# Kernel optimization log

Measured on AMD Instinct MI355X. Metric: run time of the kernel, lower is better.

## Reference

```python
import jax, jax.numpy as jnp
import numpy as np

B, C_IN, T = 16, 1, 10240
C = 256                # conv_dim_out == config.model.conv_channels
KERNEL, STRIDE, PAD = 10, 5, 0
K_STEPS = 12           # config.model.predict_steps
NEG = 10               # config.train.neg_samples
EPS = 1e-5
L_OUT = (T + 2 * PAD - KERNEL) // STRIDE + 1   # 2047


def setup_inputs() -> dict:
    key = jax.random.key(0)
    ks = jax.random.split(key, 5)
    return {
        "x": jax.random.normal(ks[0], (B, C_IN, T), jnp.float32),
        "conv_w": jax.random.normal(ks[1], (C, C_IN, KERNEL), jnp.float32) * 0.1,
        "conv_b": jnp.zeros((C,), jnp.float32),
        "bn_gamma": jnp.ones((C,), jnp.float32),
        "bn_beta": jnp.zeros((C,), jnp.float32),
        "tr_w": jax.random.normal(ks[2], (K_STEPS, C, C), jnp.float32) / np.sqrt(C).astype(np.float32),
        "tr_b": jnp.zeros((K_STEPS, C), jnp.float32),
        "perm": jax.random.permutation(ks[3], L_OUT),  # randperm over the time axis
    }


def reference(x, conv_w, conv_b, bn_gamma, bn_beta, tr_w, tr_b, perm):
    # ---- encoder: Conv1d -> ReLU -> BatchNorm1d (training-mode batch stats) ----
    h = jax.lax.conv_general_dilated(
        x, conv_w, window_strides=(STRIDE,), padding=[(PAD, PAD)],
        dimension_numbers=("NCH", "OIH", "NCH"))
    h = jax.nn.relu(h + conv_b[None, :, None])            # (B, C, L)
    mu = h.mean(axis=(0, 2), keepdims=True)
    var = h.var(axis=(0, 2), keepdims=True)               # biased, as torch BN
    h = (h - mu) * jax.lax.rsqrt(var + EPS)
    h = h * bn_gamma[None, :, None] + bn_beta[None, :, None]
    z = h.transpose(0, 2, 1)                              # (B, L, C)

    # ---- negatives: batch-roll by 1, random permutation of the time axis; detached ----
    z_negative = jax.lax.stop_gradient(jnp.roll(z, 1, axis=0)[:, perm, :])

    L = z.shape[1]
    # z_neg_full[b, i] == roll(z_neg, i, axis=0)[b] == z_neg[(b - i) % B]
    roll_idx = (jnp.arange(B)[:, None] - jnp.arange(NEG)[None, :]) % B  # (B, NEG)

    losses = []
    for k in range(1, K_STEPS + 1):
        l_len = L - k
        z_pos = z[:, k:, :]                               # (B, l, C)
        z_neg = z_negative[:, k:, :]                      # (B, l, C)
        z_neg_full = z_neg[roll_idx]                      # (B, NEG, l, C)
        W, bb = tr_w[k - 1], tr_b[k - 1]
        est_pos = (z_pos @ W + bb)[:, None]               # (B, 1, l, C)
        est_neg = z_neg_full @ W + bb                     # (B, NEG, l, C)
        estimated = jnp.concatenate([est_pos, est_neg], axis=1)        # (B, S, l, C)
        z_full = jnp.concatenate([z_pos[:, None], z_neg_full], axis=1)  # (B, S, l, C)
        f = jnp.einsum("bslc,bslc->bsl", estimated, z_full)
        # faithful to torch: flatten (b, s, l) row-major then view as (b*l, S)
        f_k = f.reshape(B * l_len, NEG + 1)
        logp = jax.nn.log_softmax(f_k, axis=1)
        losses.append(-logp.sum() / ((l_len - k) * B))

    # torch forward returns z.permute(0, 2, 1); losses returned too for baseline use
    return z.transpose(0, 2, 1), jnp.stack(losses)
```

## Files before the change

### kernel.cpp

```cpp
#include <hip/hip_runtime.h>
#include <hip/hip_bf16.h>
#include <math.h>

constexpr int B_ = 16;
constexpr int T_ = 10240;
constexpr int C_ = 256;
constexpr int KW = 10;
constexpr int L_ = 2047;
constexpr int N_ = B_ * L_;
constexpr int KSTEPS = 12;
constexpr float EPS_ = 1e-5f;
constexpr int QSTR = 32768;

typedef short bf16x8 __attribute__((ext_vector_type(8)));
typedef float f32x4  __attribute__((ext_vector_type(4)));

__global__ __launch_bounds__(256) void stats_wt_kernel(
    const float* __restrict__ x, const float* __restrict__ cw, const float* __restrict__ cb,
    float* __restrict__ ssum, float* __restrict__ ssq,
    const float* __restrict__ tw, __hip_bfloat16* __restrict__ Wt)
{
    __shared__ float smem[64 * 65];
    const int bid = blockIdx.x;
    if (bid < 256) {
        const int b  = bid & 15;
        const int l0 = (bid >> 4) * 128;
        const int cnt = min(128, L_ - l0);
        const int c = threadIdx.x;
        float* xs = smem;
        const float* xb = x + (size_t)b * T_;
        for (int i = threadIdx.x; i < cnt * 5 + 5; i += 256) xs[i] = xb[l0 * 5 + i];
        float w[KW];
#pragma unroll
        for (int j = 0; j < KW; ++j) w[j] = cw[c * KW + j];
        const float bias = cb[c];
        __syncthreads();
        float s = 0.f, s2 = 0.f;
        for (int dl = 0; dl < cnt; ++dl) {
            float v = bias;
#pragma unroll
            for (int j = 0; j < KW; ++j) v = fmaf(xs[dl * 5 + j], w[j], v);
            v = fmaxf(v, 0.f);
            s += v;
            s2 = fmaf(v, v, s2);
        }
        atomicAdd(&ssum[c], s);
        atomicAdd(&ssq[c], s2);
    } else {
        const int idx = bid - 256;
        const int k  = idx >> 4;
        const int c0 = ((idx & 15) >> 2) * 64, j0 = (idx & 3) * 64;
        float (*tile)[65] = (float(*)[65])smem;
        for (int i = threadIdx.x; i < 64 * 64; i += 256) {
            int c = i >> 6, j = i & 63;
            tile[c][j] = tw[((size_t)k * C_ + (c0 + c)) * C_ + j0 + j];
        }
        __syncthreads();
        for (int i = threadIdx.x; i < 64 * 64; i += 256) {
            int j = i >> 6, c = i & 63;
            Wt[((size_t)k * C_ + (j0 + j)) * C_ + c0 + c] = __float2bfloat16(tile[c][j]);
        }
    }
}

__global__ void bn_finalize_kernel(const float* __restrict__ ssum, const float* __restrict__ ssq,
                                   const float* __restrict__ gamma, const float* __restrict__ beta,
                                   float* __restrict__ scale, float* __restrict__ shift)
{
    int c = threadIdx.x;
    const float inv_n = 1.0f / (float)N_;
    float mu  = ssum[c] * inv_n;
    float var = ssq[c] * inv_n - mu * mu;
    float sc  = gamma[c] * rsqrtf(var + EPS_);
    scale[c] = sc;
    shift[c] = beta[c] - mu * sc;
}

__global__ __launch_bounds__(256) void conv_norm_kernel(
    const float* __restrict__ x, const float* __restrict__ cw, const float* __restrict__ cb,
    const float* __restrict__ scale, const float* __restrict__ shift,
    __hip_bfloat16* __restrict__ Zb, float* __restrict__ out0)
{
    const int b  = blockIdx.y;
    const int l0 = blockIdx.x * 32;
    const int cnt = min(32, L_ - l0);
    const int c = threadIdx.x;
    __shared__ float xs[32 * 5 + 8];
    __shared__ float zt[32][257];
    const float* xb = x + (size_t)b * T_;
    for (int i = threadIdx.x; i < cnt * 5 + 5; i += 256) xs[i] = xb[l0 * 5 + i];
    float w[KW];
#pragma unroll
    for (int j = 0; j < KW; ++j) w[j] = cw[c * KW + j];
    const float bias = cb[c];
    const float sc = scale[c], sh = shift[c];
    __syncthreads();
    for (int dl = 0; dl < cnt; ++dl) {
        float v = bias;
#pragma unroll
        for (int j = 0; j < KW; ++j) v = fmaf(xs[dl * 5 + j], w[j], v);
        v = fmaxf(v, 0.f);
        float z = fmaf(v, sc, sh);
        Zb[((size_t)(b * L_ + l0 + dl)) * C_ + c] = __float2bfloat16(z);
        zt[dl][c] = z;
    }
    __syncthreads();
    const int lq  = threadIdx.x & 31;
    const int cr0 = threadIdx.x >> 5;
    if (lq < cnt) {
#pragma unroll
        for (int i = 0; i < 32; ++i) {
            int cr = cr0 * 32 + i;
            out0[((size_t)(b * C_ + cr)) * L_ + l0 + lq] = zt[lq][cr];
        }
    }
}

__global__ __launch_bounds__(256, 2) void qmfma_kernel(
    const __hip_bfloat16* __restrict__ Zb, const __hip_bfloat16* __restrict__ Wt,
    const float* __restrict__ tb, float* __restrict__ qt)
{
    const int k   = blockIdx.y;
    const int grp = blockIdx.x;
    const __hip_bfloat16* __restrict__ Wk = Wt + (size_t)k * C_ * C_;

    __shared__ __hip_bfloat16 zs[2][32 * 256];
    __shared__ float qacc[4][256];

    const int tid  = threadIdx.x;
    const int lane = tid & 63, wave = tid >> 6;
    const int n16  = lane & 15, quad = lane >> 4;
    const int sw   = n16 & 7;

    bf16x8 wfrag[4][8];
    {
        const __hip_bfloat16* wb = Wk + ((size_t)(64 * wave + n16)) * C_ + quad * 8;
#pragma unroll
        for (int ct = 0; ct < 4; ++ct)
#pragma unroll
            for (int it = 0; it < 8; ++it)
                wfrag[ct][it] = *(const bf16x8*)(wb + ct * 16 * C_ + it * 32);
    }
    float4 bias4[4];
#pragma unroll
    for (int ct = 0; ct < 4; ++ct)
        bias4[ct] = *(const float4*)(tb + k * C_ + 64 * wave + ct * 16 + quad * 4);

    const int row0 = grp * 8 * 32;
    float4 greg[4];

#pragma unroll
    for (int i = 0; i < 4; ++i) {
        int chunk = tid + i * 256;
        int r = chunk >> 5;
        int rg = row0 + r; if (rg > N_ - 1) rg = N_ - 1;
        greg[i] = *(const float4*)(Zb + (size_t)rg * C_ + (chunk & 31) * 8);
    }
#pragma unroll
    for (int i = 0; i < 4; ++i) {
        int chunk = tid + i * 256;
        int r = chunk >> 5, j = chunk & 31;
        *(float4*)((__hip_bfloat16*)zs[0] + r * 256 + (j ^ (r & 7)) * 8) = greg[i];
    }
    __syncthreads();

    for (int t = 0; t < 8; ++t) {
        const int p = t & 1;

        if (t < 7) {
            int r0 = row0 + (t + 1) * 32;
#pragma unroll
            for (int i = 0; i < 4; ++i) {
                int chunk = tid + i * 256;
                int r = chunk >> 5;
                int rg = r0 + r; if (rg > N_ - 1) rg = N_ - 1;
                greg[i] = *(const float4*)(Zb + (size_t)rg * C_ + (chunk & 31) * 8);
            }
        }

        f32x4 acc[2][4];
#pragma unroll
        for (int rt = 0; rt < 2; ++rt)
#pragma unroll
            for (int ct = 0; ct < 4; ++ct) acc[rt][ct] = f32x4{0.f, 0.f, 0.f, 0.f};

        const __hip_bfloat16* zsp = (const __hip_bfloat16*)zs[p];
#pragma unroll
        for (int it = 0; it < 8; ++it) {
            const int js = (it * 4 + quad) ^ sw;
            bf16x8 zf0 = *(const bf16x8*)(zsp + n16 * 256 + js * 8);
            bf16x8 zf1 = *(const bf16x8*)(zsp + (n16 + 16) * 256 + js * 8);
#pragma unroll
            for (int ct = 0; ct < 4; ++ct) {
                acc[0][ct] = __builtin_amdgcn_mfma_f32_16x16x32_bf16(
                    wfrag[ct][it], zf0, acc[0][ct], 0, 0, 0);
                acc[1][ct] = __builtin_amdgcn_mfma_f32_16x16x32_bf16(
                    wfrag[ct][it], zf1, acc[1][ct], 0, 0, 0);
            }
        }

#pragma unroll
        for (int rt = 0; rt < 2; ++rt) {
            const int row = rt * 16 + n16;
            float s = 0.f;
#pragma unroll
            for (int ct = 0; ct < 4; ++ct) {
                const int j  = 8 * wave + 2 * ct + (quad >> 1);
                const char* zp = (const char*)zsp + row * 512 + ((j ^ sw) << 4) + (quad & 1) * 8;
                uint2 zz = *(const uint2*)zp;
                float z0 = __uint_as_float(zz.x << 16);
                float z1 = __uint_as_float(zz.x & 0xffff0000u);
                float z2 = __uint_as_float(zz.y << 16);
                float z3 = __uint_as_float(zz.y & 0xffff0000u);
                s = fmaf(acc[rt][ct][0] + bias4[ct].x, z0, s);
                s = fmaf(acc[rt][ct][1] + bias4[ct].y, z1, s);
                s = fmaf(acc[rt][ct][2] + bias4[ct].z, z2, s);
                s = fmaf(acc[rt][ct][3] + bias4[ct].w, z3, s);
            }
            s += __shfl_xor(s, 16);
            s += __shfl_xor(s, 32);
            if (lane < 16) qacc[wave][t * 32 + row] = s;
        }

        if (t < 7) {
#pragma unroll
            for (int i = 0; i < 4; ++i) {
                int chunk = tid + i * 256;
                int r = chunk >> 5, j = chunk & 31;
                *(float4*)((__hip_bfloat16*)zs[1 - p] + r * 256 + (j ^ (r & 7)) * 8) = greg[i];
            }
        }
        __syncthreads();
    }

    {
        int r  = tid;
        int rg = row0 + r;
        if (rg < N_) {
            float qv = qacc[0][r] + qacc[1][r] + qacc[2][r] + qacc[3][r];
            int b = rg / L_;
            int l = rg - b * L_;
            qt[(size_t)k * QSTR + (l << 4) + b] = qv;
        }
    }
}

__global__ __launch_bounds__(256) void loss_kernel(
    const float* __restrict__ qt, const int* __restrict__ perm, float* __restrict__ lacc)
{
    const int k = blockIdx.y + 1;
    const float* qk = qt + (size_t)(k - 1) * QSTR;
    const int nval = B_ * (L_ - k);
    const int idx = blockIdx.x * 256 + threadIdx.x;

    float contrib = 0.f;
    if (idx < nval) {
        int b = idx & 15;
        int l = k + (idx >> 4);
        float f0 = qk[(l << 4) | b];
        int pl = perm[l];
        const float* qn = qk + ((size_t)pl << 4);
        float f[10];
#pragma unroll
        for (int n = 0; n < 10; ++n) f[n] = qn[(b + 15 - n) & 15];
        float m = f0;
#pragma unroll
        for (int i = 0; i < 10; ++i) m = fmaxf(m, f[i]);
        float se = expf(f0 - m), fs = f0;
#pragma unroll
        for (int i = 0; i < 10; ++i) { se += expf(f[i] - m); fs += f[i]; }
        contrib = 11.f * (m + logf(se)) - fs;
    }

    __shared__ float red[4];
#pragma unroll
    for (int off = 32; off > 0; off >>= 1) contrib += __shfl_down(contrib, off);
    const int lane = threadIdx.x & 63;
    const int wave = threadIdx.x >> 6;
    if (lane == 0) red[wave] = contrib;
    __syncthreads();
    if (threadIdx.x == 0) atomicAdd(&lacc[k - 1], red[0] + red[1] + red[2] + red[3]);
}

__global__ void finalize_loss_kernel(const float* __restrict__ lacc, float* __restrict__ out1)
{
    int k = threadIdx.x;
    if (k < KSTEPS) {
        float div = (float)((L_ - 2 * (k + 1)) * B_);
        out1[k] = lacc[k] / div;
    }
}

extern "C" void kernel_launch(void* const* d_in, const int* in_sizes, int n_in,
                              void* d_out, int out_size, void* d_ws, size_t ws_size,
                              hipStream_t stream)
{
    const float* x     = (const float*)d_in[0];
    const float* cw    = (const float*)d_in[1];
    const float* cb    = (const float*)d_in[2];
    const float* gamma = (const float*)d_in[3];
    const float* beta  = (const float*)d_in[4];
    const float* tw    = (const float*)d_in[5];
    const float* tb    = (const float*)d_in[6];
    const int*   perm  = (const int*)d_in[7];

    float* out0 = (float*)d_out;
    float* out1 = out0 + (size_t)B_ * C_ * L_;

    char* ws = (char*)d_ws;
    __hip_bfloat16* Zb = (__hip_bfloat16*)ws;   ws += (size_t)N_ * C_ * 2;
    __hip_bfloat16* Wt = (__hip_bfloat16*)ws;   ws += (size_t)KSTEPS * C_ * C_ * 2;
    float* qt    = (float*)ws;                  ws += (size_t)KSTEPS * QSTR * 4;
    float* ssum  = (float*)ws;                  ws += C_ * 4;
    float* ssq   = (float*)ws;                  ws += C_ * 4;
    float* lacc  = (float*)ws;                  ws += 64 * 4;
    float* scale = (float*)ws;                  ws += C_ * 4;
    float* shift = (float*)ws;                  ws += C_ * 4;

    hipMemsetAsync(ssum, 0, (C_ + C_ + 64) * sizeof(float), stream);

    stats_wt_kernel<<<448, 256, 0, stream>>>(x, cw, cb, ssum, ssq, tw, Wt);
    bn_finalize_kernel<<<1, 256, 0, stream>>>(ssum, ssq, gamma, beta, scale, shift);

    dim3 gcv(64, 16);
    conv_norm_kernel<<<gcv, 256, 0, stream>>>(x, cw, cb, scale, shift, Zb, out0);

    dim3 gq(128, KSTEPS);
    qmfma_kernel<<<gq, 256, 0, stream>>>(Zb, Wt, tb, qt);

    dim3 gl(128, KSTEPS);
    loss_kernel<<<gl, 256, 0, stream>>>(qt, perm, lacc);
    finalize_loss_kernel<<<1, 64, 0, stream>>>(lacc, out1);
}
```

Before: 191.9 us.

## Fold BN finalize into conv, vectorize x loads and output stores, double GEMM grid

Removes the separate BN finalize launch by computing scale and shift per channel inside the conv/normalize kernel. Both conv passes now read input samples as float4 straight from global memory into registers instead of staging them through shared memory. The transposed fp32 output is written as float4 stores from a channel-major shared tile. The q-projection GEMM grid is doubled with half the rows per block, giving more blocks for occupancy at the cost of reloading the weight fragments twice as often.

```diff
diff --git a/kernel.cpp b/kernel.cpp
--- a/kernel.cpp
+++ b/kernel.cpp
@@ -25,24 +25,30 @@
     if (bid < 256) {
         const int b  = bid & 15;
         const int l0 = (bid >> 4) * 128;
-        const int cnt = min(128, L_ - l0);
-        const int c = threadIdx.x;
-        float* xs = smem;
-        const float* xb = x + (size_t)b * T_;
-        for (int i = threadIdx.x; i < cnt * 5 + 5; i += 256) xs[i] = xb[l0 * 5 + i];
+        const int c  = threadIdx.x;
         float w[KW];
 #pragma unroll
         for (int j = 0; j < KW; ++j) w[j] = cw[c * KW + j];
         const float bias = cb[c];
-        __syncthreads();
+        const float* xg = x + (size_t)b * T_ + l0 * 5;
+        const int xlim = 10236 - 5 * l0;
         float s = 0.f, s2 = 0.f;
-        for (int dl = 0; dl < cnt; ++dl) {
-            float v = bias;
-#pragma unroll
-            for (int j = 0; j < KW; ++j) v = fmaf(xs[dl * 5 + j], w[j], v);
-            v = fmaxf(v, 0.f);
-            s += v;
-            s2 = fmaf(v, v, s2);
+        for (int ci = 0; ci < 16; ++ci) {
+            float xr[48];
+#pragma unroll
+            for (int u = 0; u < 12; ++u) {
+                int o = min(40 * ci + 4 * u, xlim);
+                *(float4*)&xr[u * 4] = *(const float4*)(xg + o);
+            }
+#pragma unroll
+            for (int i = 0; i < 8; ++i) {
+                int l = l0 + ci * 8 + i;
+                float v = bias;
+#pragma unroll
+                for (int j = 0; j < KW; ++j) v = fmaf(xr[5 * i + j], w[j], v);
+                v = fmaxf(v, 0.f);
+                if (l < L_) { s += v; s2 = fmaf(v, v, s2); }
+            }
         }
         atomicAdd(&ssum[c], s);
         atomicAdd(&ssq[c], s2);
@@ -63,55 +69,67 @@
     }
 }
 
-__global__ void bn_finalize_kernel(const float* __restrict__ ssum, const float* __restrict__ ssq,
-                                   const float* __restrict__ gamma, const float* __restrict__ beta,
-                                   float* __restrict__ scale, float* __restrict__ shift)
-{
-    int c = threadIdx.x;
-    const float inv_n = 1.0f / (float)N_;
-    float mu  = ssum[c] * inv_n;
-    float var = ssq[c] * inv_n - mu * mu;
-    float sc  = gamma[c] * rsqrtf(var + EPS_);
-    scale[c] = sc;
-    shift[c] = beta[c] - mu * sc;
-}
-
 __global__ __launch_bounds__(256) void conv_norm_kernel(
     const float* __restrict__ x, const float* __restrict__ cw, const float* __restrict__ cb,
-    const float* __restrict__ scale, const float* __restrict__ shift,
+    const float* __restrict__ ssum, const float* __restrict__ ssq,
+    const float* __restrict__ gamma, const float* __restrict__ beta,
     __hip_bfloat16* __restrict__ Zb, float* __restrict__ out0)
 {
     const int b  = blockIdx.y;
     const int l0 = blockIdx.x * 32;
-    const int cnt = min(32, L_ - l0);
-    const int c = threadIdx.x;
-    __shared__ float xs[32 * 5 + 8];
-    __shared__ float zt[32][257];
-    const float* xb = x + (size_t)b * T_;
-    for (int i = threadIdx.x; i < cnt * 5 + 5; i += 256) xs[i] = xb[l0 * 5 + i];
+    const int c  = threadIdx.x;
+    __shared__ float zt2[256][33];
+
     float w[KW];
 #pragma unroll
     for (int j = 0; j < KW; ++j) w[j] = cw[c * KW + j];
     const float bias = cb[c];
-    const float sc = scale[c], sh = shift[c];
+    const float inv_n = 1.0f / (float)N_;
+    const float mu  = ssum[c] * inv_n;
+    const float var = ssq[c] * inv_n - mu * mu;
+    const float sc  = gamma[c] * rsqrtf(var + EPS_);
+    const float sh  = beta[c] - mu * sc;
+
+    const float* xg = x + (size_t)b * T_ + l0 * 5;
+    const int xlim = 10236 - 5 * l0;
+#pragma unroll
+    for (int ci = 0; ci < 4; ++ci) {
+        float xr[48];
+#pragma unroll
+        for (int u = 0; u < 12; ++u) {
+            int o = min(40 * ci + 4 * u, xlim);
+            *(float4*)&xr[u * 4] = *(const float4*)(xg + o);
+        }
+#pragma unroll
+        for (int i = 0; i < 8; ++i) {
+            int l = l0 + ci * 8 + i;
+            float v = bias;
+#pragma unroll
+            for (int j = 0; j < KW; ++j) v = fmaf(xr[5 * i + j], w[j], v);
+            v = fmaxf(v, 0.f);
+            float z = fmaf(v, sc, sh);
+            if (l < L_) Zb[((size_t)(b * L_ + l)) * C_ + c] = __float2bfloat16(z);
+            zt2[c][ci * 8 + i] = z;
+        }
+    }
     __syncthreads();
-    for (int dl = 0; dl < cnt; ++dl) {
-        float v = bias;
-#pragma unroll
-        for (int j = 0; j < KW; ++j) v = fmaf(xs[dl * 5 + j], w[j], v);
-        v = fmaxf(v, 0.f);
-        float z = fmaf(v, sc, sh);
-        Zb[((size_t)(b * L_ + l0 + dl)) * C_ + c] = __float2bfloat16(z);
-        zt[dl][c] = z;
-    }
-    __syncthreads();
-    const int lq  = threadIdx.x & 31;
-    const int cr0 = threadIdx.x >> 5;
-    if (lq < cnt) {
-#pragma unroll
-        for (int i = 0; i < 32; ++i) {
-            int cr = cr0 * 32 + i;
-            out0[((size_t)(b * C_ + cr)) * L_ + l0 + lq] = zt[lq][cr];
+    const int q4 = threadIdx.x & 7;
+    const int cb0 = threadIdx.x >> 3;
+    const int lb = l0 + q4 * 4;
+#pragma unroll
+    for (int i = 0; i < 8; ++i) {
+        int cr = cb0 + 32 * i;
+        float4 v;
+        v.x = zt2[cr][q4 * 4 + 0];
+        v.y = zt2[cr][q4 * 4 + 1];
+        v.z = zt2[cr][q4 * 4 + 2];
+        v.w = zt2[cr][q4 * 4 + 3];
+        float* op = out0 + ((size_t)(b * C_ + cr)) * L_ + lb;
+        if (lb + 3 < L_) *(float4*)op = v;
+        else {
+            if (lb     < L_) op[0] = v.x;
+            if (lb + 1 < L_) op[1] = v.y;
+            if (lb + 2 < L_) op[2] = v.z;
         }
     }
 }
@@ -125,7 +143,7 @@
     const __hip_bfloat16* __restrict__ Wk = Wt + (size_t)k * C_ * C_;
 
     __shared__ __hip_bfloat16 zs[2][32 * 256];
-    __shared__ float qacc[4][256];
+    __shared__ float qacc[4][128];
 
     const int tid  = threadIdx.x;
     const int lane = tid & 63, wave = tid >> 6;
@@ -146,7 +164,7 @@
     for (int ct = 0; ct < 4; ++ct)
         bias4[ct] = *(const float4*)(tb + k * C_ + 64 * wave + ct * 16 + quad * 4);
 
-    const int row0 = grp * 8 * 32;
+    const int row0 = grp * 128;
     float4 greg[4];
 
 #pragma unroll
@@ -164,10 +182,10 @@
     }
     __syncthreads();
 
-    for (int t = 0; t < 8; ++t) {
+    for (int t = 0; t < 4; ++t) {
         const int p = t & 1;
 
-        if (t < 7) {
+        if (t < 3) {
             int r0 = row0 + (t + 1) * 32;
 #pragma unroll
             for (int i = 0; i < 4; ++i) {
@@ -222,7 +240,7 @@
             if (lane < 16) qacc[wave][t * 32 + row] = s;
         }
 
-        if (t < 7) {
+        if (t < 3) {
 #pragma unroll
             for (int i = 0; i < 4; ++i) {
                 int chunk = tid + i * 256;
@@ -233,11 +251,10 @@
         __syncthreads();
     }
 
-    {
-        int r  = tid;
-        int rg = row0 + r;
+    if (tid < 128) {
+        int rg = row0 + tid;
         if (rg < N_) {
-            float qv = qacc[0][r] + qacc[1][r] + qacc[2][r] + qacc[3][r];
+            float qv = qacc[0][tid] + qacc[1][tid] + qacc[2][tid] + qacc[3][tid];
             int b = rg / L_;
             int l = rg - b * L_;
             qt[(size_t)k * QSTR + (l << 4) + b] = qv;
@@ -314,18 +331,15 @@
     float* ssum  = (float*)ws;                  ws += C_ * 4;
     float* ssq   = (float*)ws;                  ws += C_ * 4;
     float* lacc  = (float*)ws;                  ws += 64 * 4;
-    float* scale = (float*)ws;                  ws += C_ * 4;
-    float* shift = (float*)ws;                  ws += C_ * 4;
 
     hipMemsetAsync(ssum, 0, (C_ + C_ + 64) * sizeof(float), stream);
 
     stats_wt_kernel<<<448, 256, 0, stream>>>(x, cw, cb, ssum, ssq, tw, Wt);
-    bn_finalize_kernel<<<1, 256, 0, stream>>>(ssum, ssq, gamma, beta, scale, shift);
 
     dim3 gcv(64, 16);
-    conv_norm_kernel<<<gcv, 256, 0, stream>>>(x, cw, cb, scale, shift, Zb, out0);
-
-    dim3 gq(128, KSTEPS);
+    conv_norm_kernel<<<gcv, 256, 0, stream>>>(x, cw, cb, ssum, ssq, gamma, beta, Zb, out0);
+
+    dim3 gq(256, KSTEPS);
     qmfma_kernel<<<gq, 256, 0, stream>>>(Zb, Wt, tb, qt);
 
     dim3 gl(128, KSTEPS);
```

Result: slower. 213.5 us (+11.2%).
